# Kernel optimization log

Measured on AMD Instinct MI355X. Metric: run time of the kernel, lower is better.

Reference implementation:

```python
import jax, jax.numpy as jnp
import numpy as np

HIDDEN = 1024
INTER = 2048
NUM_EXPERTS = 8
TOP_K = 2
GROUP_SIZE = 128
TOKENS = 4096


def _dequant_int4(packed, scale, group_size):
    # packed: [E, N, K//2] ints in [0,256) holding two uint4 nibbles (low | high<<4)
    # scale:  [E, N, K//group_size] float32
    E, N, Kh = packed.shape
    K = 2 * Kh
    low = packed & 0xF
    high = (packed >> 4) & 0xF
    # interleave: even K positions = low nibble, odd = high nibble
    q = jnp.stack([low, high], axis=-1).reshape(E, N, K) - 8  # int4 values in [-8,7]
    q = q.astype(jnp.float32).reshape(E, N, K // group_size, group_size)
    w = q * scale[..., None]
    return w.reshape(E, N, K)


def setup_inputs() -> dict:
    key = jax.random.key(0)
    k1, k2, k3, k4, k5, k6 = jax.random.split(key, 6)
    x = jax.random.normal(k1, (TOKENS, HIDDEN), dtype=jnp.float32)
    router_w = jax.random.normal(k2, (NUM_EXPERTS, HIDDEN), dtype=jnp.float32) * 0.02
    w1 = jax.random.randint(k3, (NUM_EXPERTS, 2 * INTER, HIDDEN // 2), 0, 256, dtype=jnp.int32)
    w1_scale = jax.random.uniform(k4, (NUM_EXPERTS, 2 * INTER, HIDDEN // GROUP_SIZE), dtype=jnp.float32) * 0.05
    w2 = jax.random.randint(k5, (NUM_EXPERTS, HIDDEN, INTER // 2), 0, 256, dtype=jnp.int32)
    w2_scale = jax.random.uniform(k6, (NUM_EXPERTS, HIDDEN, INTER // GROUP_SIZE), dtype=jnp.float32) * 0.05
    return {"x": x, "router_w": router_w, "w1": w1, "w1_scale": w1_scale, "w2": w2, "w2_scale": w2_scale}


def reference(x, router_w, w1, w1_scale, w2, w2_scale):
    # Router: topk then softmax over the top-k logits
    scores = x @ router_w.T                                 # [T, E]
    top_w, top_i = jax.lax.top_k(scores, TOP_K)             # [T, K]
    top_w = jax.nn.softmax(top_w, axis=-1).astype(jnp.float32)

    # Dequantize int4 grouped weights once
    w1_deq = _dequant_int4(w1, w1_scale, GROUP_SIZE)        # [E, 2I, H]
    w2_deq = _dequant_int4(w2, w2_scale, GROUP_SIZE)        # [E, H, I]

    out = jnp.zeros_like(x)
    for e in range(NUM_EXPERTS):
        # per-token routing weight for expert e (0 if not routed)
        ge = jnp.sum(top_w * (top_i == e), axis=-1)         # [T]
        h = x @ w1_deq[e].T                                  # [T, 2I]
        gate, up = h[:, :INTER], h[:, INTER:]
        a = jax.nn.silu(gate) * up                           # SwiGLU
        y = a @ w2_deq[e].T                                  # [T, H]
        out = out + ge[:, None] * y
    return out
```

## Files before the change

kernel.cpp:

```cpp
#include <hip/hip_runtime.h>
#include <hip/hip_bf16.h>

#define HIDDEN 1024
#define INTER 2048
#define NE 8
#define GS 128
#define TOKENS 4096
#define MAXROWS 9216
#define MAXTILES 72

typedef __bf16 bf16x8 __attribute__((ext_vector_type(8)));
typedef float f32x4 __attribute__((ext_vector_type(4)));

#define OFF_TOPKI 0u
#define OFF_TOPKW 32768u
#define OFF_CTRL  65536u
#define OFF_TOK   66048u
#define OFF_SLOT  102912u
#define OFF_TILE  135680u
#define OFF_XG    139776u
#define OFF_A     19014144u
#define OFF_W1D   56762880u
#define OFF_W2D   123871744u

__device__ __forceinline__ unsigned short f2bf(float f) {
  union { float f; unsigned int u; } v; v.f = f;
  unsigned int r = (v.u + 0x7FFFu + ((v.u >> 16) & 1u)) >> 16;
  return (unsigned short)r;
}
__device__ __forceinline__ float bf2f(unsigned int u) {
  union { unsigned int u; float f; } v; v.u = u << 16;
  return v.f;
}
__device__ __forceinline__ unsigned int pack2(unsigned short lo, unsigned short hi) {
  return (unsigned int)lo | ((unsigned int)hi << 16);
}

typedef const __attribute__((address_space(1))) unsigned int GAS;
typedef __attribute__((address_space(3))) unsigned int LAS;
__device__ __forceinline__ void gload16(const unsigned short* g, unsigned short* l) {
  __builtin_amdgcn_global_load_lds((GAS*)g, (LAS*)l, 16, 0, 0);
}


__global__ __launch_bounds__(256) void k_prep(const float* __restrict__ x,
    const float* __restrict__ rw, int* __restrict__ topki, float* __restrict__ topkw,
    const int* __restrict__ w1, const float* __restrict__ w1s,
    unsigned short* __restrict__ w1d) {
  int bid = blockIdx.x, tid = threadIdx.x;
  if (bid >= 1024) {
    int gid = (bid - 1024) * 256 + tid;
    int i4 = gid * 4;
    int r = i4 >> 9;
    int i = i4 & 511;
    float s = w1s[r * 8 + (i >> 6)];
    int4 p = *reinterpret_cast<const int4*>(w1 + (size_t)i4);
    int pv[4] = { p.x, p.y, p.z, p.w };
    uint4 o; unsigned int ov[4];
#pragma unroll
    for (int j = 0; j < 4; j++) {
      float lo = (float)((pv[j] & 15) - 8) * s;
      float hi = (float)(((pv[j] >> 4) & 15) - 8) * s;
      ov[j] = pack2(f2bf(lo), f2bf(hi));
    }
    o.x = ov[0]; o.y = ov[1]; o.z = ov[2]; o.w = ov[3];
    *reinterpret_cast<uint4*>(w1d + ((size_t)r << 10) + 2 * i) = o;
    return;
  }
  int wave = tid >> 6, lane = tid & 63;
  int t = bid * 4 + wave;
  float acc[NE];
#pragma unroll
  for (int e = 0; e < NE; e++) acc[e] = 0.f;
  const float* xr = x + (size_t)t * HIDDEN;
  for (int i = lane; i < HIDDEN; i += 64) {
    float xv = xr[i];
#pragma unroll
    for (int e = 0; e < NE; e++) acc[e] += xv * rw[e * HIDDEN + i];
  }
#pragma unroll
  for (int e = 0; e < NE; e++) {
    float v = acc[e];
    for (int off = 32; off > 0; off >>= 1) v += __shfl_down(v, off, 64);
    acc[e] = v;
  }
  if (lane == 0) {
    int b0 = 0; float s0 = acc[0];
#pragma unroll
    for (int e = 1; e < NE; e++) if (acc[e] > s0) { s0 = acc[e]; b0 = e; }
    int b1 = -1; float s1 = -3.0e38f;
#pragma unroll
    for (int e = 0; e < NE; e++) if (e != b0 && acc[e] > s1) { s1 = acc[e]; b1 = e; }
    float w0 = 1.f / (1.f + __expf(s1 - s0));
    topki[t * 2] = b0; topki[t * 2 + 1] = b1;
    topkw[t * 2] = w0; topkw[t * 2 + 1] = 1.f - w0;
  }
}

__global__ __launch_bounds__(256) void k_route2(const int* __restrict__ topki,
    int* __restrict__ ctrl, int* __restrict__ tok, int* __restrict__ slots,
    int* __restrict__ tilemap) {
  __shared__ int h[NE], off[NE], cnt[NE];
  int tid = threadIdx.x;
  if (tid < NE) h[tid] = 0;
  __syncthreads();
  for (int i = tid; i < TOKENS * 2; i += 256) atomicAdd(&h[topki[i]], 1);
  __syncthreads();
  if (tid == 0) {
    int run = 0, t = 0;
    for (int e = 0; e < NE; e++) {
      int c = h[e];
      ctrl[e] = c; ctrl[16 + e] = run; off[e] = run;
      int pc = (c + 127) & ~127;
      for (int mt = 0; mt < (pc >> 7); mt++) tilemap[t++] = (e << 20) | (run + mt * 128);
      run += pc;
    }
    ctrl[24] = run; ctrl[25] = t;
  }
  __syncthreads();
#pragma unroll
  for (int e = 0; e < NE; e++) {
    int c = h[e], pc = (c + 127) & ~127;
    for (int i = c + tid; i < pc; i += 256) tok[off[e] + i] = -1;
  }
  if (tid < NE) cnt[tid] = off[tid];
  __syncthreads();
  for (int i = tid; i < TOKENS * 2; i += 256) {
    int e = topki[i];
    int p = atomicAdd(&cnt[e], 1);
    tok[p] = i >> 1;
    slots[i] = p;
  }
}

__global__ __launch_bounds__(256) void k_gather(const float* __restrict__ x,
    const int* __restrict__ ctrl, const int* __restrict__ tok,
    unsigned short* __restrict__ xg) {
  int s = blockIdx.x;
  if (s >= ctrl[24]) return;
  int t = tok[s];
  int c = threadIdx.x * 4;
  unsigned short* dst = xg + (size_t)s * HIDDEN + c;
  if (t < 0) {
    uint2 z; z.x = 0u; z.y = 0u;
    *reinterpret_cast<uint2*>(dst) = z;
  } else {
    float4 v = *reinterpret_cast<const float4*>(x + (size_t)t * HIDDEN + c);
    uint2 o;
    o.x = pack2(f2bf(v.x), f2bf(v.y));
    o.y = pack2(f2bf(v.z), f2bf(v.w));
    *reinterpret_cast<uint2*>(dst) = o;
  }
}

__global__ __launch_bounds__(256) void k_gemm1x(
    const unsigned short* __restrict__ xg, const unsigned short* __restrict__ w1d,
    const int* __restrict__ ctrl, const int* __restrict__ tilemap,
    unsigned short* __restrict__ a_out,
    const int* __restrict__ w2, const float* __restrict__ w2s,
    unsigned short* __restrict__ w2d) {
  __shared__ unsigned short sA[128 * 64];
  __shared__ unsigned short sBg[64 * 64];
  __shared__ unsigned short sBu[64 * 64];
  int bid = blockIdx.x, tid = threadIdx.x;
  if (bid >= 2304) {
    int gid = (bid - 2304) * 256 + tid;
    int i4 = gid * 4;
    int r = i4 >> 10;
    int i = i4 & 1023;
    float s = w2s[r * 16 + (i >> 6)];
    int4 p = *reinterpret_cast<const int4*>(w2 + (size_t)i4);
    int pv[4] = { p.x, p.y, p.z, p.w };
    uint4 o; unsigned int ov[4];
#pragma unroll
    for (int j = 0; j < 4; j++) {
      float lo = (float)((pv[j] & 15) - 8) * s;
      float hi = (float)(((pv[j] >> 4) & 15) - 8) * s;
      ov[j] = pack2(f2bf(lo), f2bf(hi));
    }
    o.x = ov[0]; o.y = ov[1]; o.z = ov[2]; o.w = ov[3];
    *reinterpret_cast<uint4*>(w2d + ((size_t)r << 11) + 2 * i) = o;
    return;
  }
  int nt = bid & 31, tile = bid >> 5;
  if (tile >= ctrl[25]) return;
  int tm = tilemap[tile];
  int e = tm >> 20, row0 = tm & 0xFFFFF;
  int n0 = nt * 64;
  int wave = tid >> 6, lane = tid & 63;
  int ln = lane & 15, quad = lane >> 4;
  int wr = (wave & 1) * 64, wc = (wave >> 1) * 32;

  const unsigned short* gA[4];
  const unsigned short* gBg[2];
  const unsigned short* gBu[2];
#pragma unroll
  for (int j = 0; j < 4; j++) {
    int slot = tid + 256 * j, row = slot >> 3;
    int col = ((slot & 7) ^ (row & 7)) * 8;
    gA[j] = xg + (size_t)(row0 + row) * HIDDEN + col;
  }
#pragma unroll
  for (int j = 0; j < 2; j++) {
    int slot = tid + 256 * j, row = slot >> 3;
    int col = ((slot & 7) ^ (row & 7)) * 8;
    gBg[j] = w1d + ((size_t)e * 4096 + n0 + row) * HIDDEN + col;
    gBu[j] = gBg[j] + (size_t)INTER * HIDDEN;
  }

  f32x4 aG[4][2] = {}, aU[4][2] = {};
  for (int k0 = 0; k0 < HIDDEN; k0 += 64) {
    __syncthreads();
#pragma unroll
    for (int j = 0; j < 4; j++) gload16(gA[j] + k0, sA + (tid + 256 * j) * 8);
#pragma unroll
    for (int j = 0; j < 2; j++) {
      gload16(gBg[j] + k0, sBg + (tid + 256 * j) * 8);
      gload16(gBu[j] + k0, sBu + (tid + 256 * j) * 8);
    }
    __syncthreads();
#pragma unroll
    for (int kh = 0; kh < 2; kh++) {
      bf16x8 af[4], bg[2], bu[2];
#pragma unroll
      for (int m = 0; m < 4; m++) {
        int ar = wr + m * 16 + ln;
        af[m] = *reinterpret_cast<const bf16x8*>(
            &sA[ar * 64 + ((((kh << 2) | quad)) ^ (ar & 7)) * 8]);
      }
#pragma unroll
      for (int n = 0; n < 2; n++) {
        int br = wc + n * 16 + ln;
        int c = ((((kh << 2) | quad)) ^ (br & 7)) * 8;
        bg[n] = *reinterpret_cast<const bf16x8*>(&sBg[br * 64 + c]);
        bu[n] = *reinterpret_cast<const bf16x8*>(&sBu[br * 64 + c]);
      }
#pragma unroll
      for (int m = 0; m < 4; m++)
#pragma unroll
        for (int n = 0; n < 2; n++) {
          aG[m][n] = __builtin_amdgcn_mfma_f32_16x16x32_bf16(af[m], bg[n], aG[m][n], 0, 0, 0);
          aU[m][n] = __builtin_amdgcn_mfma_f32_16x16x32_bf16(af[m], bu[n], aU[m][n], 0, 0, 0);
        }
    }
  }
#pragma unroll
  for (int m = 0; m < 4; m++)
#pragma unroll
    for (int n = 0; n < 2; n++) {
      int col = n0 + wc + n * 16 + ln;
#pragma unroll
      for (int r = 0; r < 4; r++) {
        float g = aG[m][n][r], u = aU[m][n][r];
        float act = (g / (1.f + __expf(-g))) * u;
        int row = row0 + wr + m * 16 + quad * 4 + r;
        a_out[(size_t)row * INTER + col] = f2bf(act);
      }
    }
}

__global__ __launch_bounds__(256) void k_gemm2(
    const unsigned short* __restrict__ a_in, const unsigned short* __restrict__ w2d,
    const int* __restrict__ ctrl, const int* __restrict__ tilemap,
    unsigned short* __restrict__ y) {
  __shared__ unsigned short sA[128 * 64];
  __shared__ unsigned short sB[128 * 64];
  int bid = blockIdx.x, tid = threadIdx.x;
  int nt = bid & 7, tile = bid >> 3;
  if (tile >= ctrl[25]) return;
  int tm = tilemap[tile];
  int e = tm >> 20, row0 = tm & 0xFFFFF;
  int n0 = nt * 128;
  int wave = tid >> 6, lane = tid & 63;
  int ln = lane & 15, quad = lane >> 4;
  int wr = (wave & 1) * 64, wc = (wave >> 1) * 64;

  const unsigned short* gA[4];
  const unsigned short* gB[4];
#pragma unroll
  for (int j = 0; j < 4; j++) {
    int slot = tid + 256 * j, row = slot >> 3;
    int col = ((slot & 7) ^ (row & 7)) * 8;
    gA[j] = a_in + (size_t)(row0 + row) * INTER + col;
    gB[j] = w2d + ((size_t)e * 1024 + n0 + row) * INTER + col;
  }

  f32x4 acc[4][4] = {};
  for (int k0 = 0; k0 < INTER; k0 += 64) {
    __syncthreads();
#pragma unroll
    for (int j = 0; j < 4; j++) {
      gload16(gA[j] + k0, sA + (tid + 256 * j) * 8);
      gload16(gB[j] + k0, sB + (tid + 256 * j) * 8);
    }
    __syncthreads();
#pragma unroll
    for (int kh = 0; kh < 2; kh++) {
      bf16x8 af[4], bf_[4];
#pragma unroll
      for (int m = 0; m < 4; m++) {
        int ar = wr + m * 16 + ln;
        af[m] = *reinterpret_cast<const bf16x8*>(
            &sA[ar * 64 + ((((kh << 2) | quad)) ^ (ar & 7)) * 8]);
      }
#pragma unroll
      for (int n = 0; n < 4; n++) {
        int br = wc + n * 16 + ln;
        bf_[n] = *reinterpret_cast<const bf16x8*>(
            &sB[br * 64 + ((((kh << 2) | quad)) ^ (br & 7)) * 8]);
      }
#pragma unroll
      for (int m = 0; m < 4; m++)
#pragma unroll
        for (int n = 0; n < 4; n++)
          acc[m][n] = __builtin_amdgcn_mfma_f32_16x16x32_bf16(af[m], bf_[n], acc[m][n], 0, 0, 0);
    }
  }
#pragma unroll
  for (int m = 0; m < 4; m++)
#pragma unroll
    for (int n = 0; n < 4; n++) {
      int col = n0 + wc + n * 16 + ln;
#pragma unroll
      for (int r = 0; r < 4; r++) {
        int row = row0 + wr + m * 16 + quad * 4 + r;
        y[(size_t)row * HIDDEN + col] = f2bf(acc[m][n][r]);
      }
    }
}

__global__ __launch_bounds__(256) void k_combine(const unsigned short* __restrict__ y,
    const int* __restrict__ slots, const float* __restrict__ topkw,
    float* __restrict__ out) {
  int t = blockIdx.x;
  int c = threadIdx.x * 4;
  int s0 = slots[t * 2], s1 = slots[t * 2 + 1];
  float g0 = topkw[t * 2], g1 = topkw[t * 2 + 1];
  uint2 va = *reinterpret_cast<const uint2*>(y + (size_t)s0 * HIDDEN + c);
  uint2 vb = *reinterpret_cast<const uint2*>(y + (size_t)s1 * HIDDEN + c);
  float4 o;
  o.x = g0 * bf2f(va.x & 0xffffu) + g1 * bf2f(vb.x & 0xffffu);
  o.y = g0 * bf2f(va.x >> 16)     + g1 * bf2f(vb.x >> 16);
  o.z = g0 * bf2f(va.y & 0xffffu) + g1 * bf2f(vb.y & 0xffffu);
  o.w = g0 * bf2f(va.y >> 16)     + g1 * bf2f(vb.y >> 16);
  *reinterpret_cast<float4*>(out + (size_t)t * HIDDEN + c) = o;
}

extern "C" void kernel_launch(void* const* d_in, const int* in_sizes, int n_in,
                              void* d_out, int out_size, void* d_ws, size_t ws_size,
                              hipStream_t stream) {
  const float* x   = (const float*)d_in[0];
  const float* rw  = (const float*)d_in[1];
  const int*   w1  = (const int*)d_in[2];
  const float* w1s = (const float*)d_in[3];
  const int*   w2  = (const int*)d_in[4];
  const float* w2s = (const float*)d_in[5];
  float* out = (float*)d_out;
  char* ws = (char*)d_ws;

  int*   topki = (int*)(ws + OFF_TOPKI);
  float* topkw = (float*)(ws + OFF_TOPKW);
  int*   ctrl  = (int*)(ws + OFF_CTRL);
  int*   tok   = (int*)(ws + OFF_TOK);
  int*   slots = (int*)(ws + OFF_SLOT);
  int*   tilemap = (int*)(ws + OFF_TILE);
  unsigned short* xg  = (unsigned short*)(ws + OFF_XG);
  unsigned short* a   = (unsigned short*)(ws + OFF_A);
  unsigned short* w1d = (unsigned short*)(ws + OFF_W1D);
  unsigned short* w2d = (unsigned short*)(ws + OFF_W2D);

  k_prep<<<1024 + 16384, 256, 0, stream>>>(x, rw, topki, topkw, w1, w1s, w1d);
  k_route2<<<1, 256, 0, stream>>>(topki, ctrl, tok, slots, tilemap);
  k_gather<<<MAXROWS, 256, 0, stream>>>(x, ctrl, tok, xg);
  k_gemm1x<<<2304 + 8192, 256, 0, stream>>>(xg, w1d, ctrl, tilemap, a, w2, w2s, w2d);
  k_gemm2<<<8 * MAXTILES, 256, 0, stream>>>(a, w2d, ctrl, tilemap, xg );
  k_combine<<<TOKENS, 256, 0, stream>>>(xg, slots, topkw, out);
}
```

Measured before the change: 351.4 us.

## Move w2 dequant into prep kernel and halve GEMM K-tile to 32

Moves the w2 int4 dequantization blocks out of the gemm1 launch and into the prep kernel, so gemm1 carries only GEMM tiles. Both GEMM kernels shrink their K step from 64 to 32, with a new XOR swizzle for the 32-wide shared tiles. The smaller tiles cut LDS use per block, which may allow more resident blocks. In exchange the loops run twice as many iterations, each paying two barriers for half the MFMA work.

```diff
diff --git a/kernel.cpp b/kernel.cpp
--- a/kernel.cpp
+++ b/kernel.cpp
@@ -46,8 +46,29 @@
 __global__ __launch_bounds__(256) void k_prep(const float* __restrict__ x,
     const float* __restrict__ rw, int* __restrict__ topki, float* __restrict__ topkw,
     const int* __restrict__ w1, const float* __restrict__ w1s,
-    unsigned short* __restrict__ w1d) {
+    unsigned short* __restrict__ w1d,
+    const int* __restrict__ w2, const float* __restrict__ w2s,
+    unsigned short* __restrict__ w2d) {
   int bid = blockIdx.x, tid = threadIdx.x;
+  if (bid >= 17408) {
+    int gid = (bid - 17408) * 256 + tid;
+    int i4 = gid * 4;
+    int r = i4 >> 10;
+    int i = i4 & 1023;
+    float s = w2s[r * 16 + (i >> 6)];
+    int4 p = *reinterpret_cast<const int4*>(w2 + (size_t)i4);
+    int pv[4] = { p.x, p.y, p.z, p.w };
+    uint4 o; unsigned int ov[4];
+#pragma unroll
+    for (int j = 0; j < 4; j++) {
+      float lo = (float)((pv[j] & 15) - 8) * s;
+      float hi = (float)(((pv[j] >> 4) & 15) - 8) * s;
+      ov[j] = pack2(f2bf(lo), f2bf(hi));
+    }
+    o.x = ov[0]; o.y = ov[1]; o.z = ov[2]; o.w = ov[3];
+    *reinterpret_cast<uint4*>(w2d + ((size_t)r << 11) + 2 * i) = o;
+    return;
+  }
   if (bid >= 1024) {
     int gid = (bid - 1024) * 256 + tid;
     int i4 = gid * 4;
@@ -153,35 +174,14 @@
   }
 }
 
-__global__ __launch_bounds__(256) void k_gemm1x(
+__global__ __launch_bounds__(256) void k_gemm1(
     const unsigned short* __restrict__ xg, const unsigned short* __restrict__ w1d,
     const int* __restrict__ ctrl, const int* __restrict__ tilemap,
-    unsigned short* __restrict__ a_out,
-    const int* __restrict__ w2, const float* __restrict__ w2s,
-    unsigned short* __restrict__ w2d) {
-  __shared__ unsigned short sA[128 * 64];
-  __shared__ unsigned short sBg[64 * 64];
-  __shared__ unsigned short sBu[64 * 64];
+    unsigned short* __restrict__ a_out) {
+  __shared__ unsigned short sA[128 * 32];
+  __shared__ unsigned short sBg[64 * 32];
+  __shared__ unsigned short sBu[64 * 32];
   int bid = blockIdx.x, tid = threadIdx.x;
-  if (bid >= 2304) {
-    int gid = (bid - 2304) * 256 + tid;
-    int i4 = gid * 4;
-    int r = i4 >> 10;
-    int i = i4 & 1023;
-    float s = w2s[r * 16 + (i >> 6)];
-    int4 p = *reinterpret_cast<const int4*>(w2 + (size_t)i4);
-    int pv[4] = { p.x, p.y, p.z, p.w };
-    uint4 o; unsigned int ov[4];
-#pragma unroll
-    for (int j = 0; j < 4; j++) {
-      float lo = (float)((pv[j] & 15) - 8) * s;
-      float hi = (float)(((pv[j] >> 4) & 15) - 8) * s;
-      ov[j] = pack2(f2bf(lo), f2bf(hi));
-    }
-    o.x = ov[0]; o.y = ov[1]; o.z = ov[2]; o.w = ov[3];
-    *reinterpret_cast<uint4*>(w2d + ((size_t)r << 11) + 2 * i) = o;
-    return;
-  }
   int nt = bid & 31, tile = bid >> 5;
   if (tile >= ctrl[25]) return;
   int tm = tilemap[tile];
@@ -191,58 +191,45 @@
   int ln = lane & 15, quad = lane >> 4;
   int wr = (wave & 1) * 64, wc = (wave >> 1) * 32;
 
-  const unsigned short* gA[4];
-  const unsigned short* gBg[2];
-  const unsigned short* gBu[2];
-#pragma unroll
-  for (int j = 0; j < 4; j++) {
-    int slot = tid + 256 * j, row = slot >> 3;
-    int col = ((slot & 7) ^ (row & 7)) * 8;
-    gA[j] = xg + (size_t)(row0 + row) * HIDDEN + col;
-  }
-#pragma unroll
-  for (int j = 0; j < 2; j++) {
-    int slot = tid + 256 * j, row = slot >> 3;
-    int col = ((slot & 7) ^ (row & 7)) * 8;
-    gBg[j] = w1d + ((size_t)e * 4096 + n0 + row) * HIDDEN + col;
-    gBu[j] = gBg[j] + (size_t)INTER * HIDDEN;
-  }
+  int srow = tid >> 2, scblk = tid & 3;
+  int scol = (scblk ^ ((srow >> 1) & 3)) * 8;
+  const unsigned short* gA0 = xg + (size_t)(row0 + srow) * HIDDEN + scol;
+  const unsigned short* gA1 = gA0 + (size_t)64 * HIDDEN;
+  const unsigned short* gBg = w1d + ((size_t)e * 4096 + n0 + srow) * HIDDEN + scol;
+  const unsigned short* gBu = gBg + (size_t)INTER * HIDDEN;
+  unsigned short* lA0 = sA + tid * 8;
+  unsigned short* lA1 = sA + 64 * 32 + tid * 8;
+  unsigned short* lBg = sBg + tid * 8;
+  unsigned short* lBu = sBu + tid * 8;
 
   f32x4 aG[4][2] = {}, aU[4][2] = {};
-  for (int k0 = 0; k0 < HIDDEN; k0 += 64) {
+  for (int k0 = 0; k0 < HIDDEN; k0 += 32) {
     __syncthreads();
-#pragma unroll
-    for (int j = 0; j < 4; j++) gload16(gA[j] + k0, sA + (tid + 256 * j) * 8);
-#pragma unroll
-    for (int j = 0; j < 2; j++) {
-      gload16(gBg[j] + k0, sBg + (tid + 256 * j) * 8);
-      gload16(gBu[j] + k0, sBu + (tid + 256 * j) * 8);
-    }
+    gload16(gA0 + k0, lA0);
+    gload16(gA1 + k0, lA1);
+    gload16(gBg + k0, lBg);
+    gload16(gBu + k0, lBu);
     __syncthreads();
-#pragma unroll
-    for (int kh = 0; kh < 2; kh++) {
-      bf16x8 af[4], bg[2], bu[2];
-#pragma unroll
-      for (int m = 0; m < 4; m++) {
-        int ar = wr + m * 16 + ln;
-        af[m] = *reinterpret_cast<const bf16x8*>(
-            &sA[ar * 64 + ((((kh << 2) | quad)) ^ (ar & 7)) * 8]);
+    bf16x8 af[4], bg[2], bu[2];
+#pragma unroll
+    for (int m = 0; m < 4; m++) {
+      int ar = wr + m * 16 + ln;
+      af[m] = *reinterpret_cast<const bf16x8*>(&sA[ar * 32 + (quad ^ ((ar >> 1) & 3)) * 8]);
+    }
+#pragma unroll
+    for (int n = 0; n < 2; n++) {
+      int br = wc + n * 16 + ln;
+      int bo = br * 32 + (quad ^ ((br >> 1) & 3)) * 8;
+      bg[n] = *reinterpret_cast<const bf16x8*>(&sBg[bo]);
+      bu[n] = *reinterpret_cast<const bf16x8*>(&sBu[bo]);
+    }
+#pragma unroll
+    for (int m = 0; m < 4; m++)
+#pragma unroll
+      for (int n = 0; n < 2; n++) {
+        aG[m][n] = __builtin_amdgcn_mfma_f32_16x16x32_bf16(af[m], bg[n], aG[m][n], 0, 0, 0);
+        aU[m][n] = __builtin_amdgcn_mfma_f32_16x16x32_bf16(af[m], bu[n], aU[m][n], 0, 0, 0);
       }
-#pragma unroll
-      for (int n = 0; n < 2; n++) {
-        int br = wc + n * 16 + ln;
-        int c = ((((kh << 2) | quad)) ^ (br & 7)) * 8;
-        bg[n] = *reinterpret_cast<const bf16x8*>(&sBg[br * 64 + c]);
-        bu[n] = *reinterpret_cast<const bf16x8*>(&sBu[br * 64 + c]);
-      }
-#pragma unroll
-      for (int m = 0; m < 4; m++)
-#pragma unroll
-        for (int n = 0; n < 2; n++) {
-          aG[m][n] = __builtin_amdgcn_mfma_f32_16x16x32_bf16(af[m], bg[n], aG[m][n], 0, 0, 0);
-          aU[m][n] = __builtin_amdgcn_mfma_f32_16x16x32_bf16(af[m], bu[n], aU[m][n], 0, 0, 0);
-        }
-    }
   }
 #pragma unroll
   for (int m = 0; m < 4; m++)
@@ -263,8 +250,8 @@
     const unsigned short* __restrict__ a_in, const unsigned short* __restrict__ w2d,
     const int* __restrict__ ctrl, const int* __restrict__ tilemap,
     unsigned short* __restrict__ y) {
-  __shared__ unsigned short sA[128 * 64];
-  __shared__ unsigned short sB[128 * 64];
+  __shared__ unsigned short sA[128 * 32];
+  __shared__ unsigned short sB[128 * 32];
   int bid = blockIdx.x, tid = threadIdx.x;
   int nt = bid & 7, tile = bid >> 3;
   if (tile >= ctrl[25]) return;
@@ -275,46 +262,41 @@
   int ln = lane & 15, quad = lane >> 4;
   int wr = (wave & 1) * 64, wc = (wave >> 1) * 64;
 
-  const unsigned short* gA[4];
-  const unsigned short* gB[4];
-#pragma unroll
-  for (int j = 0; j < 4; j++) {
-    int slot = tid + 256 * j, row = slot >> 3;
-    int col = ((slot & 7) ^ (row & 7)) * 8;
-    gA[j] = a_in + (size_t)(row0 + row) * INTER + col;
-    gB[j] = w2d + ((size_t)e * 1024 + n0 + row) * INTER + col;
-  }
+  int srow = tid >> 2, scblk = tid & 3;
+  int scol = (scblk ^ ((srow >> 1) & 3)) * 8;
+  const unsigned short* gA0 = a_in + (size_t)(row0 + srow) * INTER + scol;
+  const unsigned short* gA1 = gA0 + (size_t)64 * INTER;
+  const unsigned short* gB0 = w2d + ((size_t)e * 1024 + n0 + srow) * INTER + scol;
+  const unsigned short* gB1 = gB0 + (size_t)64 * INTER;
+  unsigned short* lA0 = sA + tid * 8;
+  unsigned short* lA1 = sA + 64 * 32 + tid * 8;
+  unsigned short* lB0 = sB + tid * 8;
+  unsigned short* lB1 = sB + 64 * 32 + tid * 8;
 
   f32x4 acc[4][4] = {};
-  for (int k0 = 0; k0 < INTER; k0 += 64) {
+  for (int k0 = 0; k0 < INTER; k0 += 32) {
     __syncthreads();
-#pragma unroll
-    for (int j = 0; j < 4; j++) {
-      gload16(gA[j] + k0, sA + (tid + 256 * j) * 8);
-      gload16(gB[j] + k0, sB + (tid + 256 * j) * 8);
-    }
+    gload16(gA0 + k0, lA0);
+    gload16(gA1 + k0, lA1);
+    gload16(gB0 + k0, lB0);
+    gload16(gB1 + k0, lB1);
     __syncthreads();
-#pragma unroll
-    for (int kh = 0; kh < 2; kh++) {
-      bf16x8 af[4], bf_[4];
-#pragma unroll
-      for (int m = 0; m < 4; m++) {
-        int ar = wr + m * 16 + ln;
-        af[m] = *reinterpret_cast<const bf16x8*>(
-            &sA[ar * 64 + ((((kh << 2) | quad)) ^ (ar & 7)) * 8]);
-      }
-#pragma unroll
-      for (int n = 0; n < 4; n++) {
-        int br = wc + n * 16 + ln;
-        bf_[n] = *reinterpret_cast<const bf16x8*>(
-            &sB[br * 64 + ((((kh << 2) | quad)) ^ (br & 7)) * 8]);
-      }
-#pragma unroll
-      for (int m = 0; m < 4; m++)
-#pragma unroll
-        for (int n = 0; n < 4; n++)
-          acc[m][n] = __builtin_amdgcn_mfma_f32_16x16x32_bf16(af[m], bf_[n], acc[m][n], 0, 0, 0);
-    }
+    bf16x8 af[4], bf_[4];
+#pragma unroll
+    for (int m = 0; m < 4; m++) {
+      int ar = wr + m * 16 + ln;
+      af[m] = *reinterpret_cast<const bf16x8*>(&sA[ar * 32 + (quad ^ ((ar >> 1) & 3)) * 8]);
+    }
+#pragma unroll
+    for (int n = 0; n < 4; n++) {
+      int br = wc + n * 16 + ln;
+      bf_[n] = *reinterpret_cast<const bf16x8*>(&sB[br * 32 + (quad ^ ((br >> 1) & 3)) * 8]);
+    }
+#pragma unroll
+    for (int m = 0; m < 4; m++)
+#pragma unroll
+      for (int n = 0; n < 4; n++)
+        acc[m][n] = __builtin_amdgcn_mfma_f32_16x16x32_bf16(af[m], bf_[n], acc[m][n], 0, 0, 0);
   }
 #pragma unroll
   for (int m = 0; m < 4; m++)
@@ -369,10 +351,10 @@
   unsigned short* w1d = (unsigned short*)(ws + OFF_W1D);
   unsigned short* w2d = (unsigned short*)(ws + OFF_W2D);
 
-  k_prep<<<1024 + 16384, 256, 0, stream>>>(x, rw, topki, topkw, w1, w1s, w1d);
+  k_prep<<<25600, 256, 0, stream>>>(x, rw, topki, topkw, w1, w1s, w1d, w2, w2s, w2d);
   k_route2<<<1, 256, 0, stream>>>(topki, ctrl, tok, slots, tilemap);
   k_gather<<<MAXROWS, 256, 0, stream>>>(x, ctrl, tok, xg);
-  k_gemm1x<<<2304 + 8192, 256, 0, stream>>>(xg, w1d, ctrl, tilemap, a, w2, w2s, w2d);
+  k_gemm1<<<32 * MAXTILES, 256, 0, stream>>>(xg, w1d, ctrl, tilemap, a);
   k_gemm2<<<8 * MAXTILES, 256, 0, stream>>>(a, w2d, ctrl, tilemap, xg );
   k_combine<<<TOKENS, 256, 0, stream>>>(xg, slots, topkw, out);
 }
```

New measurement: 333.1 us. 1.06x faster.
